# Performance work log

Measured on AMD Instinct MI355X. Metric: run time of the kernel, lower is better.

## Reference

```python
import jax, jax.numpy as jnp
import numpy as np
from jax import lax

B, L, C = 8, 1024, 256
H = 8  # num_heads
EPS = 1e-5


def _conv_bn(img, w, gamma, beta):
    # img: [B, C_in, h, w]; w: [C_out, C_in, 3, 3]; 3x3 conv, stride 1, pad 1, no bias
    out = lax.conv_general_dilated(img, w, window_strides=(1, 1),
                                   padding=[(1, 1), (1, 1)],
                                   dimension_numbers=('NCHW', 'OIHW', 'NCHW'))
    # BatchNorm2d in train mode: per-channel batch stats over (B, h, w), biased var
    mu = out.mean(axis=(0, 2, 3), keepdims=True)
    var = out.var(axis=(0, 2, 3), keepdims=True)
    out = (out - mu) * lax.rsqrt(var + EPS)
    out = out * gamma[None, :, None, None] + beta[None, :, None, None]
    b, c, hh, ww = out.shape
    return out.reshape(b, c, hh * ww).transpose(0, 2, 1)  # b (h w) c


def setup_inputs() -> dict:
    key = jax.random.key(0)
    ks = jax.random.split(key, 10)
    s = 0.02
    inp = {
        'x': jax.random.normal(ks[0], (B, L, C), jnp.float32),
        'y': jax.random.normal(ks[1], (B, L, C), jnp.float32),
        'h': 32,
        'w': 32,
        'conv_q_w': jax.random.normal(ks[2], (C, C, 3, 3), jnp.float32) * s,
        'bn_q_g': jnp.ones((C,), jnp.float32),
        'bn_q_b': jnp.zeros((C,), jnp.float32),
        'conv_k_w': jax.random.normal(ks[3], (C, C, 3, 3), jnp.float32) * s,
        'bn_k_g': jnp.ones((C,), jnp.float32),
        'bn_k_b': jnp.zeros((C,), jnp.float32),
        'conv_v_w': jax.random.normal(ks[4], (C, C, 3, 3), jnp.float32) * s,
        'bn_v_g': jnp.ones((C,), jnp.float32),
        'bn_v_b': jnp.zeros((C,), jnp.float32),
        'Wq': jax.random.normal(ks[5], (C, C), jnp.float32) * s,
        'Wk': jax.random.normal(ks[6], (C, C), jnp.float32) * s,
        'Wv': jax.random.normal(ks[7], (C, C), jnp.float32) * s,
        'Wo': jax.random.normal(ks[8], (C, C), jnp.float32) * s,
        'bo': jnp.zeros((C,), jnp.float32),
    }
    return inp


def reference(x, y, h, w,
              conv_q_w, bn_q_g, bn_q_b,
              conv_k_w, bn_k_g, bn_k_b,
              conv_v_w, bn_v_g, bn_v_b,
              Wq, Wk, Wv, Wo, bo):
    b, t, c = x.shape
    x_img = x.transpose(0, 2, 1).reshape(b, c, h, w)
    y_img = y.transpose(0, 2, 1).reshape(b, c, h, w)

    q = _conv_bn(x_img, conv_q_w, bn_q_g, bn_q_b)  # [B, L, C]
    k = _conv_bn(y_img, conv_k_w, bn_k_g, bn_k_b)
    v = _conv_bn(y_img, conv_v_w, bn_v_g, bn_v_b)

    d = c // H
    # Linear (no bias) then split heads: b t (h d) -> b h t d
    q = (q @ Wq.T).reshape(b, -1, H, d).transpose(0, 2, 1, 3)
    k = (k @ Wk.T).reshape(b, -1, H, d).transpose(0, 2, 1, 3)
    v = (v @ Wv.T).reshape(b, -1, H, d).transpose(0, 2, 1, 3)

    scale = c ** (-0.5)  # NOTE: original scales by dim_q**-0.5, not head_dim
    attn = jax.nn.softmax(jnp.einsum('bhlk,bhtk->bhlt', q, k) * scale, axis=-1)
    out = jnp.einsum('bhlt,bhtv->bhlv', attn, v)
    out = out.transpose(0, 2, 1, 3).reshape(b, -1, c)  # b h t d -> b t (h d)
    return out @ Wo.T + bo
```

## Files before the change

kernel.cpp:

```cpp
#include <hip/hip_runtime.h>
#include <cmath>

#define BB 8
#define LLEN 1024
#define CC 256
#define NH 8
#define HD 32
#define IMG 32
#define EPSBN 1e-5f
#define QSCALE 0.0625f
#define SCLOG2E 0.09016844005556f

typedef short bf16x8 __attribute__((ext_vector_type(8)));
typedef short bf16x4 __attribute__((ext_vector_type(4)));
typedef float f32x4 __attribute__((ext_vector_type(4)));

static __device__ __forceinline__ unsigned short f2bf(float v) {
  union { float f; unsigned u; } a; a.f = v;
  unsigned r = a.u + 0x7fff + ((a.u >> 16) & 1);
  return (unsigned short)(r >> 16);
}
static __device__ __forceinline__ float bf2f(unsigned short s) {
  union { unsigned u; float f; } a; a.u = ((unsigned)s) << 16; return a.f;
}

__global__ __launch_bounds__(256) void k_prep(const float* __restrict__ x,
                                              const float* __restrict__ y,
                                              const float* __restrict__ w0,
                                              const float* __restrict__ w1,
                                              const float* __restrict__ w2,
                                              const float* __restrict__ Wo,
                                              short* __restrict__ xh,
                                              short* __restrict__ yh,
                                              short* __restrict__ Wp,
                                              short* __restrict__ Woh,
                                              short* __restrict__ Wol) {
  int bid = blockIdx.x;
  if (bid < 4096) {
    const float* s = bid >= 2048 ? y : x;
    short* d = bid >= 2048 ? yh : xh;
    size_t i = (size_t)((bid & 2047) << 8) + threadIdx.x;
    float4 v = ((const float4*)s)[i];
    bf16x4 o;
    o[0] = (short)f2bf(v.x); o[1] = (short)f2bf(v.y);
    o[2] = (short)f2bf(v.z); o[3] = (short)f2bf(v.w);
    *(bf16x4*)(d + i * 4) = o;
  } else if (bid < 4864) {
    int k = bid - 4096;
    int t = k >> 8, co = k & 255, ci = threadIdx.x;
    const float* w = t == 0 ? w0 : (t == 1 ? w1 : w2);
    const float* src = w + ((size_t)co * CC + ci) * 9;
    int cb = co >> 6, nt = (co >> 4) & 3, mmw = co & 15;
    int kcw = ci >> 5, quadw = (ci >> 3) & 3, e = ci & 7;
    int lanew = quadw * 16 + mmw;
    size_t base = ((size_t)(t * 4 + cb) * 8 + kcw) * 9;
#pragma unroll
    for (int tap = 0; tap < 9; ++tap)
      Wp[((base + tap) * 4 + nt) * 512 + lanew * 8 + e] = (short)f2bf(src[tap]);
  } else {
    int i = ((bid - 4864) << 8) + threadIdx.x;
    float v = Wo[i];
    unsigned short h = f2bf(v);
    Woh[i] = (short)h;
    Wol[i] = (short)f2bf(v - bf2f(h));
  }
}

__global__ __launch_bounds__(256, 3) void k_conv(const short* __restrict__ xh,
                                                 const short* __restrict__ yh,
                                                 const short* __restrict__ Wp,
                                                 short* __restrict__ ch,
                                                 float* __restrict__ st) {
  __shared__ __align__(16) short sI[204 * 32];
  __shared__ float sws[4][32];
  __shared__ float swq[4][32];

  int tid = threadIdx.x;
  int cb = blockIdx.x;
  int co0 = cb << 6;
  int r0 = blockIdx.y << 2;
  int z = blockIdx.z;
  int t = z >> 3, b = z & 7;
  const short* inb = (t == 0 ? xh : yh) + (size_t)b * LLEN * CC;

  int lane = tid & 63, w = tid >> 6;
  int quad = lane >> 4, mm = lane & 15;
  int wr = w & 1, wc = w >> 1;

  int pbA[4];
#pragma unroll
  for (int mt = 0; mt < 4; ++mt) {
    int sp = wr * 64 + mt * 16 + mm;
    pbA[mt] = (sp >> 5) * 34 + (sp & 31);
  }
  const int dtap[9] = {0, 1, 2, 34, 35, 36, 68, 69, 70};

  bool ivalid[4], iact[4];
  int ioff[4], sidx[4];
#pragma unroll
  for (int j = 0; j < 4; ++j) {
    int idx = tid + (j << 8);
    ivalid[j] = idx < 816;
    int sp_p = idx >> 2, cg = idx & 3;
    int pr = sp_p / 34;
    int px = sp_p - pr * 34;
    int ir = r0 - 1 + pr;
    int xx = px - 1;
    iact[j] = ivalid[j] && (ir >= 0) && (ir < IMG) && (xx >= 0) && (xx < IMG);
    ioff[j] = ((ir < 0 ? 0 : ir) * 32 + (xx < 0 ? 0 : (xx > 31 ? 31 : xx))) * CC + cg * 8;
    sidx[j] = sp_p * 32 + (((cg + (sp_p >> 1)) & 3) << 3);
  }

  const short* wlane = Wp + ((size_t)(t * 4 + cb) * 8 * 9 * 4) * 512 + lane * 8;

  f32x4 acc[4][2];
#pragma unroll
  for (int mt = 0; mt < 4; ++mt)
#pragma unroll
    for (int nt = 0; nt < 2; ++nt) acc[mt][nt] = (f32x4){0.f, 0.f, 0.f, 0.f};

  bf16x8 zerov = {0, 0, 0, 0, 0, 0, 0, 0};
  bf16x8 ipf[4];
#pragma unroll
  for (int j = 0; j < 4; ++j)
    ipf[j] = iact[j] ? *(const bf16x8*)(inb + ioff[j]) : zerov;

  bf16x8 Bw[2][2];
#pragma unroll
  for (int nt = 0; nt < 2; ++nt)
    Bw[0][nt] = *(const bf16x8*)(wlane + (size_t)(wc * 2 + nt) * 512);

#pragma unroll
  for (int kc = 0; kc < 8; ++kc) {
    int ci0 = kc << 5;
    __syncthreads();
#pragma unroll
    for (int j = 0; j < 4; ++j)
      if (ivalid[j]) *(bf16x8*)(sI + sidx[j]) = ipf[j];
    __syncthreads();
    if (kc < 7) {
#pragma unroll
      for (int j = 0; j < 4; ++j)
        ipf[j] = iact[j] ? *(const bf16x8*)(inb + ioff[j] + ci0 + 32) : zerov;
    }

#pragma unroll
    for (int tap = 0; tap < 9; ++tap) {
      const int pb = (kc + tap) & 1;
      const int nb = pb ^ 1;
      if (!(kc == 7 && tap == 8)) {
        int nkc = (tap == 8) ? kc + 1 : kc;
        int ntap = (tap == 8) ? 0 : tap + 1;
        size_t fo = (size_t)((nkc * 9 + ntap) * 4 + wc * 2) * 512;
#pragma unroll
        for (int nt = 0; nt < 2; ++nt)
          Bw[nb][nt] = *(const bf16x8*)(wlane + fo + (size_t)nt * 512);
      }
      bf16x8 Af[4];
#pragma unroll
      for (int mt = 0; mt < 4; ++mt) {
        int sp_p = pbA[mt] + dtap[tap];
        Af[mt] = *(const bf16x8*)(sI + sp_p * 32 + (((quad + (sp_p >> 1)) & 3) << 3));
      }
#pragma unroll
      for (int mt = 0; mt < 4; ++mt)
#pragma unroll
        for (int nt = 0; nt < 2; ++nt)
          acc[mt][nt] = __builtin_amdgcn_mfma_f32_16x16x32_bf16(Af[mt], Bw[pb][nt],
                                                                acc[mt][nt], 0, 0, 0);
    }
  }

  size_t tb = (size_t)t * 8192 + b * 1024 + r0 * 32;
#pragma unroll
  for (int mt = 0; mt < 4; ++mt)
#pragma unroll
    for (int nt = 0; nt < 2; ++nt)
#pragma unroll
      for (int r = 0; r < 4; ++r) {
        int sp = wr * 64 + mt * 16 + quad * 4 + r;
        ch[(tb + sp) * CC + co0 + wc * 32 + nt * 16 + mm] = (short)f2bf(acc[mt][nt][r]);
      }

  float s[2], q[2];
#pragma unroll
  for (int nt = 0; nt < 2; ++nt) {
    float ss = 0.f, qq = 0.f;
#pragma unroll
    for (int mt = 0; mt < 4; ++mt)
#pragma unroll
      for (int r = 0; r < 4; ++r) {
        float v = acc[mt][nt][r];
        ss += v;
        qq += v * v;
      }
    ss += __shfl_xor(ss, 16); ss += __shfl_xor(ss, 32);
    qq += __shfl_xor(qq, 16); qq += __shfl_xor(qq, 32);
    s[nt] = ss; q[nt] = qq;
  }
  if (quad == 0) {
#pragma unroll
    for (int nt = 0; nt < 2; ++nt) {
      sws[w][nt * 16 + mm] = s[nt];
      swq[w][nt * 16 + mm] = q[nt];
    }
  }
  __syncthreads();
  if (tid < 64) {
    int wcr = tid >> 5, cl = tid & 31;
    float S = sws[wcr * 2 + 0][cl] + sws[wcr * 2 + 1][cl];
    float Q = swq[wcr * 2 + 0][cl] + swq[wcr * 2 + 1][cl];
    atomicAdd(&st[t * 512 + co0 + tid], S);
    atomicAdd(&st[t * 512 + 256 + co0 + tid], Q);
  }
}

__global__ __launch_bounds__(256) void k_fuse(const float* __restrict__ Wq,
                                              const float* __restrict__ Wk,
                                              const float* __restrict__ Wv,
                                              const float* __restrict__ gq,
                                              const float* __restrict__ gk,
                                              const float* __restrict__ gv,
                                              const float* __restrict__ bq,
                                              const float* __restrict__ bk,
                                              const float* __restrict__ bv,
                                              const float* __restrict__ st,
                                              short* __restrict__ Wfh,
                                              short* __restrict__ Wfl,
                                              float* __restrict__ bfv) {
  int t = blockIdx.y;
  const float* W = t == 0 ? Wq : (t == 1 ? Wk : Wv);
  const float* gamma = t == 0 ? gq : (t == 1 ? gk : gv);
  const float* beta = t == 0 ? bq : (t == 1 ? bk : bv);
  int co = blockIdx.x, ci = threadIdx.x;
  float mu = st[t * 512 + ci] * (1.f / 8192.f);
  float var = st[t * 512 + 256 + ci] * (1.f / 8192.f) - mu * mu;
  float a = gamma[ci] * rsqrtf(var + EPSBN);
  float dt = beta[ci] - mu * a;
  float wv = W[co * CC + ci];
  float v = wv * a;
  unsigned short hh = f2bf(v);
  Wfh[(size_t)t * 65536 + co * CC + ci] = (short)hh;
  Wfl[(size_t)t * 65536 + co * CC + ci] = (short)f2bf(v - bf2f(hh));
  __shared__ float red[256];
  red[ci] = dt * wv;
  __syncthreads();
  for (int s2 = 128; s2 > 0; s2 >>= 1) {
    if (ci < s2) red[ci] += red[ci + s2];
    __syncthreads();
  }
  if (ci == 0) bfv[t * 256 + co] = red[0];
}

__global__ __launch_bounds__(256, 2) void k_proj(const short* __restrict__ ch,
                                                 const short* __restrict__ Wfh,
                                                 const short* __restrict__ Wfl,
                                                 const float* __restrict__ bfv,
                                                 short* __restrict__ Qh,
                                                 short* __restrict__ Kh,
                                                 short* __restrict__ Vh) {
  __shared__ __align__(16) short sT[64 * 136];
  int tid = threadIdx.x;
  int t = blockIdx.z;
  int t0 = blockIdx.x << 7;
  int co0 = blockIdx.y << 6;
  int lane = tid & 63, w = tid >> 6;
  int quad = lane >> 4, mm = lane & 15;
  int colw = co0 + w * 16;
  const short* cht = ch + (size_t)t * 8192 * CC;

  bf16x8 Bh[8], Bl[8];
  {
    const short* bh = Wfh + (size_t)t * 65536 + (size_t)(colw + mm) * CC + quad * 8;
    const short* bl = Wfl + (size_t)t * 65536 + (size_t)(colw + mm) * CC + quad * 8;
#pragma unroll
    for (int kc = 0; kc < 8; ++kc) {
      Bh[kc] = *(const bf16x8*)(bh + kc * 32);
      Bl[kc] = *(const bf16x8*)(bl + kc * 32);
    }
  }
  float bv = bfv[t * 256 + colw + mm];

  int c = colw + mm;
  int hh = c >> 5, dd = c & 31;
  int bb = t0 >> 10, lbase = t0 & 1023;
  size_t hb = (size_t)(bb * 8 + hh) * 1024;

  bf16x8 A0[8], A1[8];
  auto loadA = [&](bf16x8* dst, int g) {
    const short* a = cht + (size_t)(t0 + g * 16 + mm) * CC + quad * 8;
#pragma unroll
    for (int kc = 0; kc < 8; ++kc) dst[kc] = *(const bf16x8*)(a + kc * 32);
  };
  auto compute = [&](const bf16x8* A, int g) {
    f32x4 aH = {0.f, 0.f, 0.f, 0.f}, aL = {0.f, 0.f, 0.f, 0.f};
#pragma unroll
    for (int kc = 0; kc < 8; ++kc) {
      aH = __builtin_amdgcn_mfma_f32_16x16x32_bf16(A[kc], Bh[kc], aH, 0, 0, 0);
      aL = __builtin_amdgcn_mfma_f32_16x16x32_bf16(A[kc], Bl[kc], aL, 0, 0, 0);
    }
    if (t == 0) {
#pragma unroll
      for (int r = 0; r < 4; ++r) {
        int l = lbase + g * 16 + quad * 4 + r;
        Qh[(hb + l) * 32 + dd] = (short)f2bf((aH[r] + aL[r] + bv) * SCLOG2E);
      }
    } else if (t == 1) {
#pragma unroll
      for (int r = 0; r < 4; ++r) {
        int l = lbase + g * 16 + quad * 4 + r;
        Kh[(hb + l) * 32 + dd] = (short)f2bf(aH[r] + aL[r] + bv);
      }
    } else {
#pragma unroll
      for (int r = 0; r < 4; ++r)
        sT[(w * 16 + mm) * 136 + (g >> 2) * 64 + 16 * quad + 4 * r + (g & 3)] =
            (short)f2bf(aH[r] + aL[r] + bv);
    }
  };

  loadA(A0, 0);
#pragma unroll
  for (int g = 0; g < 8; g += 2) {
    loadA(A1, g + 1);
    compute(A0, g);
    if (g + 2 < 8) loadA(A0, g + 2);
    compute(A1, g + 1);
  }

  if (t == 2) {
    __syncthreads();
    int b = t0 >> 10, l0 = t0 & 1023;
#pragma unroll
    for (int j = 0; j < 4; ++j) {
      int idx = tid + (j << 8);
      int co = idx >> 4, tg = idx & 15;
      bf16x8 v = *(const bf16x8*)(sT + co * 136 + tg * 8);
      *(bf16x8*)(Vh + ((size_t)(b * CC) + co0 + co) * LLEN + l0 + tg * 8) = v;
    }
  }
}

__global__ __launch_bounds__(256, 2) void k_attn(const short* __restrict__ Qh,
                                                 const short* __restrict__ Kh,
                                                 const short* __restrict__ Vh,
                                                 short* __restrict__ AOh) {
  __shared__ __align__(16) short sK[2][64 * 40];
  __shared__ __align__(16) short sV[2][32 * 72];
  __shared__ __align__(16) short sP[4 * 32 * 72];

  int tid = threadIdx.x;
  int lane = tid & 63, w = tid >> 6;
  int quad = lane >> 4, mm = lane & 15;
  int bh = blockIdx.x;
  int b = bh >> 3, h = bh & 7;
  int l0 = blockIdx.y << 7;

  bf16x8 qf[2];
#pragma unroll
  for (int mf = 0; mf < 2; ++mf)
    qf[mf] = *(const bf16x8*)(Qh + ((size_t)bh * 1024 + l0 + w * 32 + mf * 16 + mm) * 32 +
                              quad * 8);

  f32x4 accO[2][2], accL[2];
#pragma unroll
  for (int mf = 0; mf < 2; ++mf) {
    accO[mf][0] = (f32x4){0.f, 0.f, 0.f, 0.f};
    accO[mf][1] = (f32x4){0.f, 0.f, 0.f, 0.f};
    accL[mf] = (f32x4){0.f, 0.f, 0.f, 0.f};
  }
  bf16x8 ones;
#pragma unroll
  for (int j = 0; j < 8; ++j) ones[j] = (short)0x3F80;

  int kt = tid >> 2, kc4 = tid & 3;
  const short* kgp = Kh + ((size_t)bh * 1024 + kt) * 32 + kc4 * 8;
  int kofs = kt * 40 + kc4 * 8;
  int vd = tid >> 3, vt8 = tid & 7;
  const short* vgp = Vh + ((size_t)(b * CC) + h * HD + vd) * LLEN + vt8 * 8;
  int vofs = vd * 72 + vt8 * 8;
  short* pw = sP + w * (32 * 72);

  bf16x8 kr = *(const bf16x8*)kgp;
  bf16x8 vr = *(const bf16x8*)vgp;
  *(bf16x8*)(sK[0] + kofs) = kr;
  *(bf16x8*)(sV[0] + vofs) = vr;
  __syncthreads();

  for (int tt = 0; tt < 16; ++tt) {
    if (tt < 15) {
      kr = *(const bf16x8*)(kgp + (size_t)(tt + 1) * 64 * 32);
      vr = *(const bf16x8*)(vgp + (tt + 1) * 64);
    }
    const short* sKc = sK[tt & 1];
    const short* sVc = sV[tt & 1];

#pragma unroll
    for (int mf = 0; mf < 2; ++mf) {
      f32x4 accS[4];
#pragma unroll
      for (int nt = 0; nt < 4; ++nt) {
        bf16x8 kf = *(const bf16x8*)(sKc + (nt * 16 + mm) * 40 + quad * 8);
        f32x4 z = {0.f, 0.f, 0.f, 0.f};
        accS[nt] = __builtin_amdgcn_mfma_f32_16x16x32_bf16(qf[mf], kf, z, 0, 0, 0);
      }
#pragma unroll
      for (int r = 0; r < 4; ++r) {
        int q = mf * 16 + quad * 4 + r;
        bf16x4 pk;
#pragma unroll
        for (int nt = 0; nt < 4; ++nt) {
          union { float f; unsigned u; } cv;
          cv.f = __builtin_exp2f(accS[nt][r]);
          pk[nt] = (short)((cv.u + 0x8000u) >> 16);
        }
        *(bf16x4*)(pw + q * 72 + mm * 4) = pk;
      }
    }

#pragma unroll
    for (int kc = 0; kc < 2; ++kc) {
      bf16x8 vf0 = *(const bf16x8*)(sVc + mm * 72 + kc * 32 + quad * 8);
      bf16x8 vf1 = *(const bf16x8*)(sVc + (16 + mm) * 72 + kc * 32 + quad * 8);
#pragma unroll
      for (int mf = 0; mf < 2; ++mf) {
        bf16x8 pf = *(const bf16x8*)(pw + (mf * 16 + mm) * 72 + kc * 32 + quad * 8);
        accL[mf] = __builtin_amdgcn_mfma_f32_16x16x32_bf16(pf, ones, accL[mf], 0, 0, 0);
        accO[mf][0] = __builtin_amdgcn_mfma_f32_16x16x32_bf16(pf, vf0, accO[mf][0], 0, 0, 0);
        accO[mf][1] = __builtin_amdgcn_mfma_f32_16x16x32_bf16(pf, vf1, accO[mf][1], 0, 0, 0);
      }
    }

    if (tt < 15) {
      __syncthreads();
      *(bf16x8*)(sK[(tt + 1) & 1] + kofs) = kr;
      *(bf16x8*)(sV[(tt + 1) & 1] + vofs) = vr;
      __syncthreads();
    }
  }

#pragma unroll
  for (int mf = 0; mf < 2; ++mf)
#pragma unroll
    for (int r = 0; r < 4; ++r) {
      float inv = __builtin_amdgcn_rcpf(accL[mf][r]);
      size_t token = (size_t)(b * LLEN) + l0 + w * 32 + mf * 16 + quad * 4 + r;
      AOh[token * CC + h * HD + mm] = (short)f2bf(accO[mf][0][r] * inv);
      AOh[token * CC + h * HD + 16 + mm] = (short)f2bf(accO[mf][1][r] * inv);
    }
}

__global__ __launch_bounds__(256, 2) void k_out(const short* __restrict__ AOh,
                                                const short* __restrict__ Woh,
                                                const short* __restrict__ Wol,
                                                const float* __restrict__ bo,
                                                float* __restrict__ out) {
  int tid = threadIdx.x;
  int t0 = blockIdx.x << 6;
  int co0 = blockIdx.y << 6;
  int lane = tid & 63, w = tid >> 6;
  int quad = lane >> 4, mm = lane & 15;
  int colw = co0 + w * 16;

  bf16x8 Bh[8], Bl[8];
  {
    const short* bh = Woh + (size_t)(colw + mm) * CC + quad * 8;
    const short* bl = Wol + (size_t)(colw + mm) * CC + quad * 8;
#pragma unroll
    for (int kc = 0; kc < 8; ++kc) {
      Bh[kc] = *(const bf16x8*)(bh + kc * 32);
      Bl[kc] = *(const bf16x8*)(bl + kc * 32);
    }
  }
  float bv = bo[colw + mm];

  bf16x8 A0[8], A1[8];
  auto loadA = [&](bf16x8* dst, int g) {
    const short* a = AOh + (size_t)(t0 + g * 16 + mm) * CC + quad * 8;
#pragma unroll
    for (int kc = 0; kc < 8; ++kc) dst[kc] = *(const bf16x8*)(a + kc * 32);
  };
  auto compute = [&](const bf16x8* A, int g) {
    f32x4 aH = {0.f, 0.f, 0.f, 0.f}, aL = {0.f, 0.f, 0.f, 0.f};
#pragma unroll
    for (int kc = 0; kc < 8; ++kc) {
      aH = __builtin_amdgcn_mfma_f32_16x16x32_bf16(A[kc], Bh[kc], aH, 0, 0, 0);
      aL = __builtin_amdgcn_mfma_f32_16x16x32_bf16(A[kc], Bl[kc], aL, 0, 0, 0);
    }
#pragma unroll
    for (int r = 0; r < 4; ++r) {
      int token = t0 + g * 16 + quad * 4 + r;
      out[(size_t)token * CC + colw + mm] = aH[r] + aL[r] + bv;
    }
  };

  loadA(A0, 0);
#pragma unroll
  for (int g = 0; g < 4; g += 2) {
    loadA(A1, g + 1);
    compute(A0, g);
    if (g + 2 < 4) loadA(A0, g + 2);
    compute(A1, g + 1);
  }
}

extern "C" void kernel_launch(void* const* d_in, const int* in_sizes, int n_in,
                              void* d_out, int out_size, void* d_ws, size_t ws_size,
                              hipStream_t stream) {
  (void)in_sizes; (void)n_in; (void)out_size; (void)ws_size;
  const float* x  = (const float*)d_in[0];
  const float* y  = (const float*)d_in[1];
  const float* wq = (const float*)d_in[4];
  const float* gq = (const float*)d_in[5];
  const float* bq = (const float*)d_in[6];
  const float* wk = (const float*)d_in[7];
  const float* gk = (const float*)d_in[8];
  const float* bk = (const float*)d_in[9];
  const float* wv = (const float*)d_in[10];
  const float* gv = (const float*)d_in[11];
  const float* bv = (const float*)d_in[12];
  const float* Wq = (const float*)d_in[13];
  const float* Wk = (const float*)d_in[14];
  const float* Wv = (const float*)d_in[15];
  const float* Wo = (const float*)d_in[16];
  const float* bo = (const float*)d_in[17];
  float* out = (float*)d_out;

  const size_t NP = (size_t)8192 * 256;
  short* xh  = (short*)d_ws;
  short* yh  = xh + NP;
  short* ch  = yh + NP;
  short* Qh  = ch + 3 * NP;
  short* Kh  = Qh + NP;
  short* Vh  = Kh + NP;
  short* AOh = Vh + NP;
  short* Wp  = AOh + NP;
  short* Wfh = Wp + (size_t)3 * 9 * 65536;
  short* Wfl = Wfh + 3 * 65536;
  short* Woh = Wfl + 3 * 65536;
  short* Wol = Woh + 65536;
  float* st  = (float*)(Wol + 65536);
  float* bfv = st + 1536;

  hipMemsetAsync(st, 0, 1536 * sizeof(float), stream);

  k_prep<<<5120, 256, 0, stream>>>(x, y, wq, wk, wv, Wo, xh, yh, Wp, Woh, Wol);

  k_conv<<<dim3(4, 8, 24), 256, 0, stream>>>(xh, yh, Wp, ch, st);

  k_fuse<<<dim3(256, 3), 256, 0, stream>>>(Wq, Wk, Wv, gq, gk, gv, bq, bk, bv,
                                           st, Wfh, Wfl, bfv);

  k_proj<<<dim3(64, 4, 3), 256, 0, stream>>>(ch, Wfh, Wfl, bfv, Qh, Kh, Vh);

  k_attn<<<dim3(64, 8), 256, 0, stream>>>(Qh, Kh, Vh, AOh);

  k_out<<<dim3(128, 4), 256, 0, stream>>>(AOh, Woh, Wol, bo, out);
}
```

Baseline: 207.4 us.

## Double-buffer conv input tile in LDS and deepen weight prefetch to three stages

```diff
diff --git a/kernel.cpp b/kernel.cpp
--- a/kernel.cpp
+++ b/kernel.cpp
@@ -71,7 +71,7 @@
                                                  const short* __restrict__ Wp,
                                                  short* __restrict__ ch,
                                                  float* __restrict__ st) {
-  __shared__ __align__(16) short sI[204 * 32];
+  __shared__ __align__(16) short sI[2][204 * 32];
   __shared__ float sws[4][32];
   __shared__ float swq[4][32];
 
@@ -125,49 +125,56 @@
   for (int j = 0; j < 4; ++j)
     ipf[j] = iact[j] ? *(const bf16x8*)(inb + ioff[j]) : zerov;
 
-  bf16x8 Bw[2][2];
-#pragma unroll
-  for (int nt = 0; nt < 2; ++nt)
-    Bw[0][nt] = *(const bf16x8*)(wlane + (size_t)(wc * 2 + nt) * 512);
+  bf16x8 Bw[4][2];
+#pragma unroll
+  for (int f = 0; f < 3; ++f)
+#pragma unroll
+    for (int nt = 0; nt < 2; ++nt)
+      Bw[f][nt] = *(const bf16x8*)(wlane + (size_t)(f * 4 + wc * 2 + nt) * 512);
+
+#pragma unroll
+  for (int j = 0; j < 4; ++j)
+    if (ivalid[j]) *(bf16x8*)(sI[0] + sidx[j]) = ipf[j];
+  __syncthreads();
 
 #pragma unroll
   for (int kc = 0; kc < 8; ++kc) {
-    int ci0 = kc << 5;
-    __syncthreads();
-#pragma unroll
-    for (int j = 0; j < 4; ++j)
-      if (ivalid[j]) *(bf16x8*)(sI + sidx[j]) = ipf[j];
-    __syncthreads();
     if (kc < 7) {
 #pragma unroll
       for (int j = 0; j < 4; ++j)
-        ipf[j] = iact[j] ? *(const bf16x8*)(inb + ioff[j] + ci0 + 32) : zerov;
-    }
+        ipf[j] = iact[j] ? *(const bf16x8*)(inb + ioff[j] + ((kc + 1) << 5)) : zerov;
+    }
+    const short* sc = sI[kc & 1];
 
 #pragma unroll
     for (int tap = 0; tap < 9; ++tap) {
-      const int pb = (kc + tap) & 1;
-      const int nb = pb ^ 1;
-      if (!(kc == 7 && tap == 8)) {
-        int nkc = (tap == 8) ? kc + 1 : kc;
-        int ntap = (tap == 8) ? 0 : tap + 1;
-        size_t fo = (size_t)((nkc * 9 + ntap) * 4 + wc * 2) * 512;
+      const int f = kc * 9 + tap;
+      if (f + 3 < 72) {
+        const int nf = f + 3;
 #pragma unroll
         for (int nt = 0; nt < 2; ++nt)
-          Bw[nb][nt] = *(const bf16x8*)(wlane + fo + (size_t)nt * 512);
+          Bw[nf & 3][nt] =
+              *(const bf16x8*)(wlane + (size_t)(nf * 4 + wc * 2 + nt) * 512);
       }
       bf16x8 Af[4];
 #pragma unroll
       for (int mt = 0; mt < 4; ++mt) {
         int sp_p = pbA[mt] + dtap[tap];
-        Af[mt] = *(const bf16x8*)(sI + sp_p * 32 + (((quad + (sp_p >> 1)) & 3) << 3));
+        Af[mt] = *(const bf16x8*)(sc + sp_p * 32 + (((quad + (sp_p >> 1)) & 3) << 3));
       }
 #pragma unroll
       for (int mt = 0; mt < 4; ++mt)
 #pragma unroll
         for (int nt = 0; nt < 2; ++nt)
-          acc[mt][nt] = __builtin_amdgcn_mfma_f32_16x16x32_bf16(Af[mt], Bw[pb][nt],
+          acc[mt][nt] = __builtin_amdgcn_mfma_f32_16x16x32_bf16(Af[mt], Bw[f & 3][nt],
                                                                 acc[mt][nt], 0, 0, 0);
+    }
+
+    if (kc < 7) {
+#pragma unroll
+      for (int j = 0; j < 4; ++j)
+        if (ivalid[j]) *(bf16x8*)(sI[(kc + 1) & 1] + sidx[j]) = ipf[j];
+      __syncthreads();
     }
   }
 
```

After: 207.5 us. Within noise of the previous version (+0.1%).
